# Performance work log

Hardware: AMD Instinct MI355X
Metric: run time of the kernel (lower is better)

## Reference

```python
import math
import jax, jax.numpy as jnp
import numpy as np

NP_, NA_ = 100000, 50000
IN_DIM = OUT_DIM = 128
H, DK = 4, 32
E_CITES, E_WRITES, E_REV = 600000, 300000, 300000


def setup_inputs() -> dict:
    key = jax.random.key(0)
    ks = jax.random.split(key, 16)
    s_in = 1.0 / math.sqrt(IN_DIM)   # ~ Linear default init scale
    s_dk = 1.0 / math.sqrt(DK)       # ~ xavier for d_k x d_k
    return {
        "h_paper": jax.random.normal(ks[0], (NP_, IN_DIM), jnp.float32),
        "h_author": jax.random.normal(ks[1], (NA_, IN_DIM), jnp.float32),
        "Wk": jax.random.normal(ks[2], (2, OUT_DIM, IN_DIM), jnp.float32) * s_in,
        "bk": jnp.zeros((2, OUT_DIM), jnp.float32),
        "Wq": jax.random.normal(ks[3], (2, OUT_DIM, IN_DIM), jnp.float32) * s_in,
        "bq": jnp.zeros((2, OUT_DIM), jnp.float32),
        "Wv": jax.random.normal(ks[4], (2, OUT_DIM, IN_DIM), jnp.float32) * s_in,
        "bv": jnp.zeros((2, OUT_DIM), jnp.float32),
        "Wa": jax.random.normal(ks[5], (2, OUT_DIM, OUT_DIM), jnp.float32) * s_in,
        "ba": jnp.zeros((2, OUT_DIM), jnp.float32),
        "rel_att": jax.random.normal(ks[6], (3, H, DK, DK), jnp.float32) * s_dk,
        "rel_msg": jax.random.normal(ks[7], (3, H, DK, DK), jnp.float32) * s_dk,
        "rel_pri": jnp.ones((3, H), jnp.float32),
        "skip": jnp.ones((2,), jnp.float32),
        "cites_src": jax.random.randint(ks[8], (E_CITES,), 0, NP_, jnp.int32),
        "cites_dst": jax.random.randint(ks[9], (E_CITES,), 0, NP_, jnp.int32),
        "writes_src": jax.random.randint(ks[10], (E_WRITES,), 0, NA_, jnp.int32),
        "writes_dst": jax.random.randint(ks[11], (E_WRITES,), 0, NP_, jnp.int32),
        "rev_src": jax.random.randint(ks[12], (E_REV,), 0, NP_, jnp.int32),
        "rev_dst": jax.random.randint(ks[13], (E_REV,), 0, NA_, jnp.int32),
    }


def _seg_softmax(scores, seg, n):
    # edge softmax normalized by destination node (DGL edge_softmax, norm_by='dst')
    m = jax.ops.segment_max(scores, seg, num_segments=n)
    e = jnp.exp(scores - m[seg])
    z = jax.ops.segment_sum(e, seg, num_segments=n)
    return e / z[seg]


def reference(h_paper, h_author, Wk, bk, Wq, bq, Wv, bv, Wa, ba,
              rel_att, rel_msg, rel_pri, skip,
              cites_src, cites_dst, writes_src, writes_dst, rev_src, rev_dst):
    sqrt_dk = math.sqrt(DK)

    def proj(h, W, b, t):
        return (h @ W[t].T + b[t]).reshape(-1, H, DK)  # [N, H, dk]

    def rel_agg(h_src, h_dst, ts, td, e, src, dst, n_dst):
        # relation-specific transforms of k and v (per-head dk x dk matmul)
        k = jnp.einsum('nhi,hij->nhj', proj(h_src, Wk, bk, ts), rel_att[e])
        v = jnp.einsum('nhi,hij->nhj', proj(h_src, Wv, bv, ts), rel_msg[e])
        q = proj(h_dst, Wq, bq, td)
        # per-edge attention logits: (q_dst . k_src) * pri / sqrt(dk)  -> [E, H]
        score = jnp.einsum('ehd,ehd->eh', q[dst], k[src]) * rel_pri[e] / sqrt_dk
        a = _seg_softmax(score, dst, n_dst)
        # weighted scatter-sum of messages to destination nodes
        return jax.ops.segment_sum(v[src] * a[:, :, None], dst, num_segments=n_dst)

    # cross_reducer='mean': average per-relation aggregates per dst node type
    t_paper = (rel_agg(h_paper, h_paper, 0, 0, 0, cites_src, cites_dst, NP_) +
               rel_agg(h_author, h_paper, 1, 0, 1, writes_src, writes_dst, NP_)) * 0.5
    t_author = rel_agg(h_paper, h_author, 0, 1, 2, rev_src, rev_dst, NA_)

    def out(t, h, nt):
        trans = t.reshape(-1, OUT_DIM) @ Wa[nt].T + ba[nt]  # dropout = identity (eval)
        alpha = jax.nn.sigmoid(skip[nt])
        return trans * alpha + h * (1.0 - alpha)

    return jnp.concatenate([out(t_paper, h_paper, 0), out(t_author, h_author, 1)], axis=0)
```

## Files before the change

### kernel.cpp

```cpp
#include <hip/hip_runtime.h>
#include <hip/hip_bf16.h>
#include <math.h>

#define NP 100000
#define NA 50000
#define DIM 128
#define NH 4
#define DKK 32
#define EC 600000
#define EW 300000
#define ER 300000
#define CAP 32
#define SCL 0.17677669529663687f

#define CDIV(a,b) (((a)+(b)-1)/(b))

typedef __attribute__((ext_vector_type(8))) short bf16x8;
typedef __attribute__((ext_vector_type(4))) float f32x4;
typedef __attribute__((ext_vector_type(2))) float f32x2;

__device__ __forceinline__ ushort f2b(float f){
  unsigned u = __float_as_uint(f);
  unsigned r = u + 0x7FFFu + ((u>>16)&1u);
  return (ushort)(r>>16);
}
__device__ __forceinline__ float blo(unsigned u){ return __uint_as_float(u<<16); }
__device__ __forceinline__ float bhi(unsigned u){ return __uint_as_float(u & 0xFFFF0000u); }

struct C2Args { const float4* in[2]; uint2* out[2]; };
__global__ void k_cast2(C2Args a){
  int s = blockIdx.y;
  int i = blockIdx.x*256 + threadIdx.x;
  float4 v = a.in[s][i];
  uint2 o;
  o.x = (unsigned)f2b(v.x) | ((unsigned)f2b(v.y)<<16);
  o.y = (unsigned)f2b(v.z) | ((unsigned)f2b(v.w)<<16);
  a.out[s][i] = o;
}

__global__ void k_zero_i(int* p, int n){
  int i = blockIdx.x*blockDim.x + threadIdx.x;
  if (i < n) p[i] = 0;
}

__global__ void k_fuse(const float* __restrict__ Wk, const float* __restrict__ bk,
                       const float* __restrict__ Wv, const float* __restrict__ bv,
                       const float* __restrict__ rel_att, const float* __restrict__ rel_msg,
                       ushort* __restrict__ Wfb_all, float* __restrict__ bfu_all){
  int rel = blockIdx.x >> 7;
  int ts = (rel==1) ? 1 : 0;
  ushort* Wfb = Wfb_all + rel*32768;
  float*  bfu = bfu_all + rel*256;
  int idx = (blockIdx.x & 127)*256 + threadIdx.x;
  int which = idx >> 14;
  int rem = idx & 16383;
  int op = rem >> 7;
  int j  = rem & 127;
  int h = op >> 5, jp = op & 31;
  const float* W  = which ? Wv : Wk;
  const float* R  = which ? rel_msg : rel_att;
  const float* Wt = W + (size_t)ts*DIM*DIM;
  const float* Re = R + (((size_t)rel*NH + h)*DKK)*DKK + jp;
  float acc = 0.f;
  #pragma unroll
  for (int i=0;i<DKK;i++) acc += Wt[(h*DKK+i)*DIM + j] * Re[(size_t)i*DKK];
  Wfb[which*16384 + op*DIM + j] = f2b(acc);
  if (idx < 256){
    int w2 = idx >> 7; int op2 = idx & 127; int h2 = op2>>5, jp2 = op2&31;
    const float* bsrc = (w2 ? bv : bk) + (size_t)ts*DIM;
    const float* R2 = (w2 ? rel_msg : rel_att) + (((size_t)rel*NH + h2)*DKK)*DKK + jp2;
    float accb = 0.f;
    #pragma unroll
    for (int i=0;i<DKK;i++) accb += bsrc[h2*DKK+i]*R2[(size_t)i*DKK];
    bfu[w2*DIM + op2] = accb;
  }
}

struct MArgs {
  const float* X[3];
  const ushort* W[3][3];
  const float* b[3][3];
  ushort* Y[3][3];
  int ystride[3][3];
  int N[3];
  int npan[3];
  int base[3];
};
__global__ __launch_bounds__(512) void k_mega(MArgs g){
  int b = blockIdx.x;
  int seg = (b >= g.base[2]) ? 2 : ((b >= g.base[1]) ? 1 : 0);
  int local = b - g.base[seg];
  int N = g.N[seg];
  int tile = local*64;
  if (tile >= N) return;
  int tid = threadIdx.x;
  int wv = tid >> 6, l = tid & 63;
  int lr = l & 15, lk = l >> 4;
  int rowg = wv >> 1, colg = wv & 1;
  int arow = tile + rowg*16 + lr;
  int ar = (arow < N) ? arow : 0;
  const float4* Ar = (const float4*)(g.X[seg] + (size_t)ar*DIM);
  bf16x8 A[4];
  #pragma unroll
  for (int kc=0;kc<4;kc++){
    float4 u = Ar[kc*8 + lk*2];
    float4 v = Ar[kc*8 + lk*2 + 1];
    bf16x8 a;
    a[0]=(short)f2b(u.x); a[1]=(short)f2b(u.y); a[2]=(short)f2b(u.z); a[3]=(short)f2b(u.w);
    a[4]=(short)f2b(v.x); a[5]=(short)f2b(v.y); a[6]=(short)f2b(v.z); a[7]=(short)f2b(v.w);
    A[kc] = a;
  }
  __shared__ __align__(16) ushort Wl[128*136];
  __shared__ __align__(16) ushort Ost[64*136];
  uint4* Wl4 = (uint4*)Wl;
  int npan = g.npan[seg];
  for (int p=0; p<npan; ++p){
    const uint4* Ws = (const uint4*)g.W[seg][p];
    #pragma unroll
    for (int i=0;i<4;i++){
      int idx = i*512 + tid;
      uint4 v = Ws[idx];
      int r = idx >> 4, c = idx & 15;
      Wl4[r*17 + c] = v;
    }
    __syncthreads();
    const float* bias = g.b[seg][p];
    #pragma unroll
    for (int ct=0; ct<4; ct++){
      int col = colg*64 + ct*16 + lr;
      f32x4 acc = {0.f,0.f,0.f,0.f};
      #pragma unroll
      for (int kc=0;kc<4;kc++){
        bf16x8 B = *(const bf16x8*)&Wl[col*136 + kc*32 + lk*8];
        acc = __builtin_amdgcn_mfma_f32_16x16x32_bf16(A[kc], B, acc, 0, 0, 0);
      }
      float bv = bias[col];
      #pragma unroll
      for (int j=0;j<4;j++)
        Ost[(rowg*16 + lk*4 + j)*136 + col] = f2b(acc[j] + bv);
    }
    __syncthreads();
    int orow = tid >> 3;
    int oseg = (tid & 7)*2;
    int grow = tile + orow;
    if (grow < N){
      uint4* dst = (uint4*)(g.Y[seg][p] + (size_t)grow*g.ystride[seg][p]);
      const uint4* s = (const uint4*)Ost;
      dst[oseg]   = s[orow*17 + oseg];
      dst[oseg+1] = s[orow*17 + oseg + 1];
    }
    __syncthreads();
  }
}

struct BArgs { const int* dst[3]; const int* src[3]; int* cnt[3]; int* slots[3]; int E[3]; int n[3]; };
__global__ void k_bucket(BArgs a){
  int r = blockIdx.y;
  int E = a.E[r], n = a.n[r];
  const int* dst = a.dst[r];
  const int* srcv = a.src[r];
  int* cnt = a.cnt[r];
  int* slots = a.slots[r];
  int g = blockIdx.x & 7;
  int sub = blockIdx.x >> 3;
  int chunk = (n + 7) >> 3;
  int lo = g*chunk;
  int hi = lo + chunk; if (hi > n) hi = n;
  int per = (E + 255) >> 8;
  per = (per + 3) & ~3;
  int e0 = sub*per;
  int e1 = e0 + per; if (e1 > E) e1 = E;
  for (int i = e0 + threadIdx.x*4; i < e1; i += 256*4){
    if (i + 4 <= e1){
      int4 d = *(const int4*)(dst + i);
      int4 s = *(const int4*)(srcv + i);
      if (d.x>=lo && d.x<hi){ int p=atomicAdd(&cnt[d.x],1); if(p<CAP) slots[(size_t)d.x*CAP+p]=s.x; }
      if (d.y>=lo && d.y<hi){ int p=atomicAdd(&cnt[d.y],1); if(p<CAP) slots[(size_t)d.y*CAP+p]=s.y; }
      if (d.z>=lo && d.z<hi){ int p=atomicAdd(&cnt[d.z],1); if(p<CAP) slots[(size_t)d.z*CAP+p]=s.z; }
      if (d.w>=lo && d.w<hi){ int p=atomicAdd(&cnt[d.w],1); if(p<CAP) slots[(size_t)d.w*CAP+p]=s.w; }
    } else {
      for (int j=i; j<e1; ++j){
        int d = dst[j];
        if (d>=lo && d<hi){ int p=atomicAdd(&cnt[d],1); if(p<CAP) slots[(size_t)d*CAP+p]=srcv[j]; }
      }
    }
  }
}

__device__ __forceinline__ void agg_step4(const unsigned* __restrict__ KV,
    const int4* __restrict__ sl4,
    int i, int deg, int nsrc, float qx, float qy, int lane,
    f32x2& av, float& z)
{
  int4 s4 = sl4[i>>2];
  int s0 = ((unsigned)s4.x < (unsigned)nsrc) ? s4.x : 0;
  int s1 = ((unsigned)s4.y < (unsigned)nsrc) ? s4.y : 0;
  int s2 = ((unsigned)s4.z < (unsigned)nsrc) ? s4.z : 0;
  int s3 = ((unsigned)s4.w < (unsigned)nsrc) ? s4.w : 0;
  bool v1 = (i+1 < deg), v2 = (i+2 < deg), v3 = (i+3 < deg);
  const unsigned* r0 = KV + (size_t)s0*128;
  const unsigned* r1 = KV + (size_t)s1*128;
  const unsigned* r2 = KV + (size_t)s2*128;
  const unsigned* r3 = KV + (size_t)s3*128;
  unsigned ku0 = r0[lane];
  unsigned ku1 = r1[lane];
  unsigned ku2 = r2[lane];
  unsigned ku3 = r3[lane];
  unsigned vu0 = r0[64 + lane];
  unsigned vu1 = r1[64 + lane];
  unsigned vu2 = r2[64 + lane];
  unsigned vu3 = r3[64 + lane];
  float p0 = qx*blo(ku0) + qy*bhi(ku0);
  float p1 = qx*blo(ku1) + qy*bhi(ku1);
  float p2 = qx*blo(ku2) + qy*bhi(ku2);
  float p3 = qx*blo(ku3) + qy*bhi(ku3);
  #pragma unroll
  for (int d=1; d<16; d<<=1){
    p0 += __shfl_xor(p0, d);
    p1 += __shfl_xor(p1, d);
    p2 += __shfl_xor(p2, d);
    p3 += __shfl_xor(p3, d);
  }
  float e0 = __expf(p0);
  float e1 = v1 ? __expf(p1) : 0.f;
  float e2 = v2 ? __expf(p2) : 0.f;
  float e3 = v3 ? __expf(p3) : 0.f;
  z += (e0+e1)+(e2+e3);
  f32x2 w0 = {blo(vu0), bhi(vu0)};
  f32x2 w1 = {blo(vu1), bhi(vu1)};
  f32x2 w2 = {blo(vu2), bhi(vu2)};
  f32x2 w3 = {blo(vu3), bhi(vu3)};
  av += (w0*e0 + w1*e1) + (w2*e2 + w3*e3);
}

struct AFArgs {
  const unsigned *QP, *QA, *KV0, *KV1, *KV2;
  const int *slots, *cnt;
  const float *pri;
  const ushort *WaP, *WaA;
  const float *baP, *baA;
  const float *hP, *hA;
  float *outP, *outA;
  const float *skip;
  int PB;
};
__global__ __launch_bounds__(512) void k_attnfin(AFArgs a){
  bool isP = (blockIdx.x < (unsigned)a.PB);
  int wbase = isP ? blockIdx.x*64 : (blockIdx.x - a.PB)*64;
  int N = isP ? NP : NA;
  int tid = threadIdx.x;
  int wid = tid >> 6;
  int lane = tid & 63;
  int h = lane >> 4;
  __shared__ float Ls[64][132];
  __shared__ int nextrow;
  if (tid == 0) nextrow = 0;
  __syncthreads();
  for (;;){
    int row;
    if (lane == 0) row = atomicAdd(&nextrow, 1);
    row = __shfl(row, 0);
    if (row >= 64) break;
    int w = wbase + row;
    if (w < N){
      f32x2 o;
      if (isP){
        unsigned qu = a.QP[(size_t)w*64 + lane];
        float qx = blo(qu), qy = bhi(qu);
        float s0f = a.pri[h]*SCL, s1f = a.pri[NH+h]*SCL;
        float qx0 = qx*s0f, qy0 = qy*s0f;
        float qx1 = qx*s1f, qy1 = qy*s1f;
        int d0 = a.cnt[w];      if (d0 > CAP) d0 = CAP;
        int d1 = a.cnt[NP + w]; if (d1 > CAP) d1 = CAP;
        const int4* sl0 = (const int4*)(a.slots + (size_t)w*CAP);
        const int4* sl1 = (const int4*)(a.slots + ((size_t)NP+w)*CAP);
        f32x2 x = {0.f,0.f}, y = {0.f,0.f};
        float zx = 0.f, zy = 0.f;
        int nmax = (d0 > d1) ? d0 : d1;
        for (int i = 0; i < nmax; i += 4){
          if (i < d0) agg_step4(a.KV0, sl0, i, d0, NP, qx0, qy0, lane, x, zx);
          if (i < d1) agg_step4(a.KV1, sl1, i, d1, NA, qx1, qy1, lane, y, zy);
        }
        float ix = (zx > 0.f) ? 1.f/zx : 0.f;
        float iy = (zy > 0.f) ? 1.f/zy : 0.f;
        o = x*ix + y*iy;
      } else {
        unsigned qu = a.QA[(size_t)w*64 + lane];
        float qx = blo(qu), qy = bhi(qu);
        float s2f = a.pri[2*NH+h]*SCL;
        float qx2 = qx*s2f, qy2 = qy*s2f;
        int d2 = a.cnt[2*NP + w]; if (d2 > CAP) d2 = CAP;
        const int4* sl2 = (const int4*)(a.slots + ((size_t)2*NP+w)*CAP);
        f32x2 r = {0.f,0.f};
        float zr = 0.f;
        for (int i = 0; i < d2; i += 4)
          agg_step4(a.KV2, sl2, i, d2, NP, qx2, qy2, lane, r, zr);
        float ir = (zr > 0.f) ? 1.f/zr : 0.f;
        o = r*ir;
      }
      *(f32x2*)&Ls[row][2*lane] = o;
    }
  }
  __syncthreads();
  const ushort* Wb  = isP ? a.WaP : a.WaA;
  const float* bias = isP ? a.baP : a.baA;
  const float* hin  = isP ? a.hP  : a.hA;
  float* out        = isP ? a.outP : a.outA;
  float scale       = isP ? 0.5f : 1.0f;
  float alpha = 1.f/(1.f + expf(-a.skip[isP ? 0 : 1]));
  float beta  = 1.f - alpha;
  int lr = lane & 15, lk = lane >> 4;
  int rowg = wid >> 1, colg = wid & 1;
  int r0loc = rowg*16;
  int c0 = colg*64;
  bf16x8 A[4];
  #pragma unroll
  for (int kc=0;kc<4;kc++){
    const float* src = &Ls[r0loc + lr][kc*32 + lk*8];
    bf16x8 aa;
    #pragma unroll
    for (int j=0;j<8;j++) aa[j] = (short)f2b(src[j]);
    A[kc] = aa;
  }
  __syncthreads();
  #pragma unroll
  for (int ct=0; ct<4; ct++){
    int col = c0 + ct*16 + lr;
    const bf16x8* Wrow = (const bf16x8*)(Wb + (size_t)col*DIM);
    f32x4 acc = {0.f,0.f,0.f,0.f};
    #pragma unroll
    for (int kc=0;kc<4;kc++)
      acc = __builtin_amdgcn_mfma_f32_16x16x32_bf16(A[kc], Wrow[kc*4+lk], acc, 0, 0, 0);
    float bv = bias[col];
    #pragma unroll
    for (int j=0;j<4;j++){
      int lrow = r0loc + lk*4 + j;
      Ls[lrow][col] = scale*acc[j] + bv;
    }
  }
  __syncthreads();
  int orow = tid >> 3;
  int ocb  = (tid & 7)*16;
  int row  = wbase + orow;
  if (row < N){
    const float4* H4 = (const float4*)hin;
    float4* O4 = (float4*)out;
    #pragma unroll
    for (int q=0;q<4;q++){
      float4 tv = *(const float4*)&Ls[orow][ocb + q*4];
      float4 hv = H4[(size_t)row*32 + (ocb>>2) + q];
      float4 o;
      o.x = alpha*tv.x + beta*hv.x;
      o.y = alpha*tv.y + beta*hv.y;
      o.z = alpha*tv.z + beta*hv.z;
      o.w = alpha*tv.w + beta*hv.w;
      O4[(size_t)row*32 + (ocb>>2) + q] = o;
    }
  }
}

extern "C" void kernel_launch(void* const* d_in, const int* in_sizes, int n_in,
                              void* d_out, int out_size, void* d_ws, size_t ws_size,
                              hipStream_t stream) {
  const float* h_paper = (const float*)d_in[0];
  const float* h_author= (const float*)d_in[1];
  const float* Wk = (const float*)d_in[2];
  const float* bk = (const float*)d_in[3];
  const float* Wq = (const float*)d_in[4];
  const float* bq = (const float*)d_in[5];
  const float* Wv = (const float*)d_in[6];
  const float* bv = (const float*)d_in[7];
  const float* Wa = (const float*)d_in[8];
  const float* ba = (const float*)d_in[9];
  const float* rel_att = (const float*)d_in[10];
  const float* rel_msg = (const float*)d_in[11];
  const float* rel_pri = (const float*)d_in[12];
  const float* skip    = (const float*)d_in[13];
  const int* cites_src = (const int*)d_in[14];
  const int* cites_dst = (const int*)d_in[15];
  const int* writes_src= (const int*)d_in[16];
  const int* writes_dst= (const int*)d_in[17];
  const int* rev_src   = (const int*)d_in[18];
  const int* rev_dst   = (const int*)d_in[19];

  ushort* qbP = (ushort*)d_ws;
  ushort* qbA = qbP + (size_t)NP*DIM;
  ushort* KV0 = qbA + (size_t)NA*DIM;
  ushort* KV1 = KV0 + (size_t)NP*256;
  ushort* KV2 = KV1 + (size_t)NA*256;
  ushort* Wqb = KV2 + (size_t)NP*256;
  ushort* Wab = Wqb + 32768;
  ushort* Wfb = Wab + 32768;
  float*  bfu = (float*)(Wfb + 3*32768);
  int* ib = (int*)(bfu + 3*256);
  const int NDST_TOT = 2*NP + NA;
  int* cnt_all   = ib;           ib += NDST_TOT;
  int* slots_all = ib;

  float* t_paper  = (float*)d_out;
  float* t_author = (float*)d_out + (size_t)NP*DIM;

  const int cntB[3] = {0, NP, 2*NP};

  {
    C2Args a;
    a.in[0]=(const float4*)Wq; a.out[0]=(uint2*)Wqb;
    a.in[1]=(const float4*)Wa; a.out[1]=(uint2*)Wab;
    k_cast2<<<dim3(32,2),256,0,stream>>>(a);
  }
  k_fuse<<<384,256,0,stream>>>(Wk, bk, Wv, bv, rel_att, rel_msg, Wfb, bfu);
  k_zero_i<<<CDIV(NDST_TOT,256),256,0,stream>>>(cnt_all, NDST_TOT);
  {
    BArgs b;
    const int* dsts[3] = {cites_dst, writes_dst, rev_dst};
    const int* srcs[3] = {cites_src, writes_src, rev_src};
    int Es[3] = {EC, EW, ER};
    int ns[3] = {NP, NP, NA};
    for (int r=0;r<3;r++){
      b.dst[r]=dsts[r]; b.src[r]=srcs[r];
      b.cnt[r]=cnt_all+cntB[r];
      b.slots[r]=slots_all+(size_t)cntB[r]*CAP;
      b.E[r]=Es[r]; b.n[r]=ns[r];
    }
    k_bucket<<<dim3(2048,3),256,0,stream>>>(b);
  }
  {
    const int T0 = CDIV(NP,64), T1 = CDIV(NA,64), T2 = CDIV(NP,64);
    MArgs m;
    m.base[0]=0; m.base[1]=T0; m.base[2]=T0+T1;
    m.X[0]=h_paper;  m.N[0]=NP; m.npan[0]=3;
    m.W[0][0]=Wqb;        m.b[0][0]=bq;        m.Y[0][0]=qbP;      m.ystride[0][0]=128;
    m.W[0][1]=Wfb;        m.b[0][1]=bfu;       m.Y[0][1]=KV0;      m.ystride[0][1]=256;
    m.W[0][2]=Wfb+16384;  m.b[0][2]=bfu+DIM;   m.Y[0][2]=KV0+128;  m.ystride[0][2]=256;
    m.X[1]=h_author; m.N[1]=NA; m.npan[1]=3;
    m.W[1][0]=Wqb+16384;        m.b[1][0]=bq+DIM;        m.Y[1][0]=qbA;      m.ystride[1][0]=128;
    m.W[1][1]=Wfb+32768;        m.b[1][1]=bfu+256;       m.Y[1][1]=KV1;      m.ystride[1][1]=256;
    m.W[1][2]=Wfb+32768+16384;  m.b[1][2]=bfu+256+DIM;   m.Y[1][2]=KV1+128;  m.ystride[1][2]=256;
    m.X[2]=h_paper;  m.N[2]=NP; m.npan[2]=2;
    m.W[2][0]=Wfb+2*32768;        m.b[2][0]=bfu+512;       m.Y[2][0]=KV2;      m.ystride[2][0]=256;
    m.W[2][1]=Wfb+2*32768+16384;  m.b[2][1]=bfu+512+DIM;   m.Y[2][1]=KV2+128;  m.ystride[2][1]=256;
    m.W[2][2]=Wfb;                m.b[2][2]=bfu;           m.Y[2][2]=KV2;      m.ystride[2][2]=256;
    k_mega<<<T0+T1+T2,512,0,stream>>>(m);
  }
  {
    const int PB = CDIV(NP,64);
    const int AB = CDIV(NA,64);
    AFArgs a;
    a.QP = (const unsigned*)qbP;  a.QA = (const unsigned*)qbA;
    a.KV0 = (const unsigned*)KV0; a.KV1 = (const unsigned*)KV1; a.KV2 = (const unsigned*)KV2;
    a.slots = slots_all; a.cnt = cnt_all;
    a.pri = rel_pri;
    a.WaP = Wab; a.WaA = Wab + 16384;
    a.baP = ba;  a.baA = ba + DIM;
    a.hP = h_paper; a.hA = h_author;
    a.outP = t_paper; a.outA = t_author;
    a.skip = skip;
    a.PB = PB;
    k_attnfin<<<PB+AB,512,0,stream>>>(a);
  }
}
```

Baseline: 327.0 us.

## Merge setup kernels and co-schedule edge bucketing with projection GEMMs

The weight cast, weight fusion and counter-zeroing kernels are combined into one launch. Edge bucketing is folded into the projection GEMM launch as extra blocks, so the atomic-bound scatter work can overlap with the MFMA projection tiles. This cuts kernel launch count and the serialization between independent stages. The cost is a larger, heterogeneous grid where bucketing blocks use 512 threads with a different edge partition, and they may compete with the GEMM blocks for CU resources.

```diff
diff --git a/kernel.cpp b/kernel.cpp
--- a/kernel.cpp
+++ b/kernel.cpp
@@ -27,56 +27,61 @@
 __device__ __forceinline__ float blo(unsigned u){ return __uint_as_float(u<<16); }
 __device__ __forceinline__ float bhi(unsigned u){ return __uint_as_float(u & 0xFFFF0000u); }
 
-struct C2Args { const float4* in[2]; uint2* out[2]; };
-__global__ void k_cast2(C2Args a){
-  int s = blockIdx.y;
-  int i = blockIdx.x*256 + threadIdx.x;
-  float4 v = a.in[s][i];
-  uint2 o;
-  o.x = (unsigned)f2b(v.x) | ((unsigned)f2b(v.y)<<16);
-  o.y = (unsigned)f2b(v.z) | ((unsigned)f2b(v.w)<<16);
-  a.out[s][i] = o;
-}
-
-__global__ void k_zero_i(int* p, int n){
-  int i = blockIdx.x*blockDim.x + threadIdx.x;
-  if (i < n) p[i] = 0;
-}
-
-__global__ void k_fuse(const float* __restrict__ Wk, const float* __restrict__ bk,
-                       const float* __restrict__ Wv, const float* __restrict__ bv,
-                       const float* __restrict__ rel_att, const float* __restrict__ rel_msg,
-                       ushort* __restrict__ Wfb_all, float* __restrict__ bfu_all){
-  int rel = blockIdx.x >> 7;
-  int ts = (rel==1) ? 1 : 0;
-  ushort* Wfb = Wfb_all + rel*32768;
-  float*  bfu = bfu_all + rel*256;
-  int idx = (blockIdx.x & 127)*256 + threadIdx.x;
-  int which = idx >> 14;
-  int rem = idx & 16383;
-  int op = rem >> 7;
-  int j  = rem & 127;
-  int h = op >> 5, jp = op & 31;
-  const float* W  = which ? Wv : Wk;
-  const float* R  = which ? rel_msg : rel_att;
-  const float* Wt = W + (size_t)ts*DIM*DIM;
-  const float* Re = R + (((size_t)rel*NH + h)*DKK)*DKK + jp;
-  float acc = 0.f;
-  #pragma unroll
-  for (int i=0;i<DKK;i++) acc += Wt[(h*DKK+i)*DIM + j] * Re[(size_t)i*DKK];
-  Wfb[which*16384 + op*DIM + j] = f2b(acc);
-  if (idx < 256){
-    int w2 = idx >> 7; int op2 = idx & 127; int h2 = op2>>5, jp2 = op2&31;
-    const float* bsrc = (w2 ? bv : bk) + (size_t)ts*DIM;
-    const float* R2 = (w2 ? rel_msg : rel_att) + (((size_t)rel*NH + h2)*DKK)*DKK + jp2;
-    float accb = 0.f;
-    #pragma unroll
-    for (int i=0;i<DKK;i++) accb += bsrc[h2*DKK+i]*R2[(size_t)i*DKK];
-    bfu[w2*DIM + op2] = accb;
-  }
-}
-
-struct MArgs {
+struct PreArgs {
+  const float4* wqin; uint2* wqout;
+  const float4* wain; uint2* waout;
+  const float *Wk, *bk, *Wv, *bv, *rel_att, *rel_msg;
+  ushort* Wfb_all; float* bfu_all;
+  int* cnt; int ncnt;
+};
+__global__ void k_pre(PreArgs a){
+  int b = blockIdx.x;
+  int tid = threadIdx.x;
+  if (b < 64){
+    const float4* in = (b < 32) ? a.wqin : a.wain;
+    uint2* out = (b < 32) ? a.wqout : a.waout;
+    int i = (b & 31)*256 + tid;
+    float4 v = in[i];
+    uint2 o;
+    o.x = (unsigned)f2b(v.x) | ((unsigned)f2b(v.y)<<16);
+    o.y = (unsigned)f2b(v.z) | ((unsigned)f2b(v.w)<<16);
+    out[i] = o;
+  } else if (b < 448){
+    int fb = b - 64;
+    int rel = fb >> 7;
+    int ts = (rel==1) ? 1 : 0;
+    ushort* Wfb = a.Wfb_all + rel*32768;
+    float*  bfu = a.bfu_all + rel*256;
+    int idx = (fb & 127)*256 + tid;
+    int which = idx >> 14;
+    int rem = idx & 16383;
+    int op = rem >> 7;
+    int j  = rem & 127;
+    int h = op >> 5, jp = op & 31;
+    const float* W  = which ? a.Wv : a.Wk;
+    const float* R  = which ? a.rel_msg : a.rel_att;
+    const float* Wt = W + (size_t)ts*DIM*DIM;
+    const float* Re = R + (((size_t)rel*NH + h)*DKK)*DKK + jp;
+    float acc = 0.f;
+    #pragma unroll
+    for (int i=0;i<DKK;i++) acc += Wt[(h*DKK+i)*DIM + j] * Re[(size_t)i*DKK];
+    Wfb[which*16384 + op*DIM + j] = f2b(acc);
+    if (idx < 256){
+      int w2 = idx >> 7; int op2 = idx & 127; int h2 = op2>>5, jp2 = op2&31;
+      const float* bsrc = (w2 ? a.bv : a.bk) + (size_t)ts*DIM;
+      const float* R2 = (w2 ? a.rel_msg : a.rel_att) + (((size_t)rel*NH + h2)*DKK)*DKK + jp2;
+      float accb = 0.f;
+      #pragma unroll
+      for (int i=0;i<DKK;i++) accb += bsrc[h2*DKK+i]*R2[(size_t)i*DKK];
+      bfu[w2*DIM + op2] = accb;
+    }
+  } else {
+    int i = (b - 448)*256 + tid;
+    if (i < a.ncnt) a.cnt[i] = 0;
+  }
+}
+
+struct CArgs {
   const float* X[3];
   const ushort* W[3][3];
   const float* b[3][3];
@@ -85,15 +90,57 @@
   int N[3];
   int npan[3];
   int base[3];
+  int MT;
+  const int* dst[3];
+  const int* src[3];
+  int* cnt[3];
+  int* slots[3];
+  int E[3];
+  int n[3];
 };
-__global__ __launch_bounds__(512) void k_mega(MArgs g){
+__global__ __launch_bounds__(512) void k_combo(CArgs g){
+  int tid = threadIdx.x;
+  if ((int)blockIdx.x >= g.MT){
+    int bb = blockIdx.x - g.MT;
+    int r = bb >> 10;
+    int lb = bb & 1023;
+    int E = g.E[r], n = g.n[r];
+    const int* dst = g.dst[r];
+    const int* srcv = g.src[r];
+    int* cnt = g.cnt[r];
+    int* slots = g.slots[r];
+    int grp = lb & 7;
+    int sub = lb >> 3;
+    int chunk = (n + 7) >> 3;
+    int lo = grp*chunk;
+    int hi = lo + chunk; if (hi > n) hi = n;
+    int per = (E + 127) >> 7;
+    per = (per + 3) & ~3;
+    int e0 = sub*per;
+    int e1 = e0 + per; if (e1 > E) e1 = E;
+    for (int i = e0 + tid*4; i < e1; i += 512*4){
+      if (i + 4 <= e1){
+        int4 d = *(const int4*)(dst + i);
+        int4 s = *(const int4*)(srcv + i);
+        if (d.x>=lo && d.x<hi){ int p=atomicAdd(&cnt[d.x],1); if(p<CAP) slots[(size_t)d.x*CAP+p]=s.x; }
+        if (d.y>=lo && d.y<hi){ int p=atomicAdd(&cnt[d.y],1); if(p<CAP) slots[(size_t)d.y*CAP+p]=s.y; }
+        if (d.z>=lo && d.z<hi){ int p=atomicAdd(&cnt[d.z],1); if(p<CAP) slots[(size_t)d.z*CAP+p]=s.z; }
+        if (d.w>=lo && d.w<hi){ int p=atomicAdd(&cnt[d.w],1); if(p<CAP) slots[(size_t)d.w*CAP+p]=s.w; }
+      } else {
+        for (int j=i; j<e1; ++j){
+          int d = dst[j];
+          if (d>=lo && d<hi){ int p=atomicAdd(&cnt[d],1); if(p<CAP) slots[(size_t)d*CAP+p]=srcv[j]; }
+        }
+      }
+    }
+    return;
+  }
   int b = blockIdx.x;
   int seg = (b >= g.base[2]) ? 2 : ((b >= g.base[1]) ? 1 : 0);
   int local = b - g.base[seg];
   int N = g.N[seg];
   int tile = local*64;
   if (tile >= N) return;
-  int tid = threadIdx.x;
   int wv = tid >> 6, l = tid & 63;
   int lr = l & 15, lk = l >> 4;
   int rowg = wv >> 1, colg = wv & 1;
@@ -120,8 +167,7 @@
     for (int i=0;i<4;i++){
       int idx = i*512 + tid;
       uint4 v = Ws[idx];
-      int r = idx >> 4, c = idx & 15;
-      Wl4[r*17 + c] = v;
+      Wl4[(idx>>4)*17 + (idx&15)] = v;
     }
     __syncthreads();
     const float* bias = g.b[seg][p];
@@ -150,40 +196,6 @@
       dst[oseg+1] = s[orow*17 + oseg + 1];
     }
     __syncthreads();
-  }
-}
-
-struct BArgs { const int* dst[3]; const int* src[3]; int* cnt[3]; int* slots[3]; int E[3]; int n[3]; };
-__global__ void k_bucket(BArgs a){
-  int r = blockIdx.y;
-  int E = a.E[r], n = a.n[r];
-  const int* dst = a.dst[r];
-  const int* srcv = a.src[r];
-  int* cnt = a.cnt[r];
-  int* slots = a.slots[r];
-  int g = blockIdx.x & 7;
-  int sub = blockIdx.x >> 3;
-  int chunk = (n + 7) >> 3;
-  int lo = g*chunk;
-  int hi = lo + chunk; if (hi > n) hi = n;
-  int per = (E + 255) >> 8;
-  per = (per + 3) & ~3;
-  int e0 = sub*per;
-  int e1 = e0 + per; if (e1 > E) e1 = E;
-  for (int i = e0 + threadIdx.x*4; i < e1; i += 256*4){
-    if (i + 4 <= e1){
-      int4 d = *(const int4*)(dst + i);
-      int4 s = *(const int4*)(srcv + i);
-      if (d.x>=lo && d.x<hi){ int p=atomicAdd(&cnt[d.x],1); if(p<CAP) slots[(size_t)d.x*CAP+p]=s.x; }
-      if (d.y>=lo && d.y<hi){ int p=atomicAdd(&cnt[d.y],1); if(p<CAP) slots[(size_t)d.y*CAP+p]=s.y; }
-      if (d.z>=lo && d.z<hi){ int p=atomicAdd(&cnt[d.z],1); if(p<CAP) slots[(size_t)d.z*CAP+p]=s.z; }
-      if (d.w>=lo && d.w<hi){ int p=atomicAdd(&cnt[d.w],1); if(p<CAP) slots[(size_t)d.w*CAP+p]=s.w; }
-    } else {
-      for (int j=i; j<e1; ++j){
-        int d = dst[j];
-        if (d>=lo && d<hi){ int p=atomicAdd(&cnt[d],1); if(p<CAP) slots[(size_t)d*CAP+p]=srcv[j]; }
-      }
-    }
   }
 }
 
@@ -403,44 +415,43 @@
   const int cntB[3] = {0, NP, 2*NP};
 
   {
-    C2Args a;
-    a.in[0]=(const float4*)Wq; a.out[0]=(uint2*)Wqb;
-    a.in[1]=(const float4*)Wa; a.out[1]=(uint2*)Wab;
-    k_cast2<<<dim3(32,2),256,0,stream>>>(a);
-  }
-  k_fuse<<<384,256,0,stream>>>(Wk, bk, Wv, bv, rel_att, rel_msg, Wfb, bfu);
-  k_zero_i<<<CDIV(NDST_TOT,256),256,0,stream>>>(cnt_all, NDST_TOT);
+    PreArgs p;
+    p.wqin = (const float4*)Wq; p.wqout = (uint2*)Wqb;
+    p.wain = (const float4*)Wa; p.waout = (uint2*)Wab;
+    p.Wk = Wk; p.bk = bk; p.Wv = Wv; p.bv = bv;
+    p.rel_att = rel_att; p.rel_msg = rel_msg;
+    p.Wfb_all = Wfb; p.bfu_all = bfu;
+    p.cnt = cnt_all; p.ncnt = NDST_TOT;
+    k_pre<<<448 + CDIV(NDST_TOT,256),256,0,stream>>>(p);
+  }
   {
-    BArgs b;
+    const int T0 = CDIV(NP,64), T1 = CDIV(NA,64), T2 = CDIV(NP,64);
+    const int MT = T0+T1+T2;
+    CArgs c;
+    c.base[0]=0; c.base[1]=T0; c.base[2]=T0+T1; c.MT = MT;
+    c.X[0]=h_paper;  c.N[0]=NP; c.npan[0]=3;
+    c.W[0][0]=Wqb;        c.b[0][0]=bq;        c.Y[0][0]=qbP;      c.ystride[0][0]=128;
+    c.W[0][1]=Wfb;        c.b[0][1]=bfu;       c.Y[0][1]=KV0;      c.ystride[0][1]=256;
+    c.W[0][2]=Wfb+16384;  c.b[0][2]=bfu+DIM;   c.Y[0][2]=KV0+128;  c.ystride[0][2]=256;
+    c.X[1]=h_author; c.N[1]=NA; c.npan[1]=3;
+    c.W[1][0]=Wqb+16384;        c.b[1][0]=bq+DIM;        c.Y[1][0]=qbA;      c.ystride[1][0]=128;
+    c.W[1][1]=Wfb+32768;        c.b[1][1]=bfu+256;       c.Y[1][1]=KV1;      c.ystride[1][1]=256;
+    c.W[1][2]=Wfb+32768+16384;  c.b[1][2]=bfu+256+DIM;   c.Y[1][2]=KV1+128;  c.ystride[1][2]=256;
+    c.X[2]=h_paper;  c.N[2]=NP; c.npan[2]=2;
+    c.W[2][0]=Wfb+2*32768;        c.b[2][0]=bfu+512;       c.Y[2][0]=KV2;      c.ystride[2][0]=256;
+    c.W[2][1]=Wfb+2*32768+16384;  c.b[2][1]=bfu+512+DIM;   c.Y[2][1]=KV2+128;  c.ystride[2][1]=256;
+    c.W[2][2]=Wfb;                c.b[2][2]=bfu;           c.Y[2][2]=KV2;      c.ystride[2][2]=256;
     const int* dsts[3] = {cites_dst, writes_dst, rev_dst};
     const int* srcs[3] = {cites_src, writes_src, rev_src};
     int Es[3] = {EC, EW, ER};
     int ns[3] = {NP, NP, NA};
     for (int r=0;r<3;r++){
-      b.dst[r]=dsts[r]; b.src[r]=srcs[r];
-      b.cnt[r]=cnt_all+cntB[r];
-      b.slots[r]=slots_all+(size_t)cntB[r]*CAP;
-      b.E[r]=Es[r]; b.n[r]=ns[r];
-    }
-    k_bucket<<<dim3(2048,3),256,0,stream>>>(b);
-  }
-  {
-    const int T0 = CDIV(NP,64), T1 = CDIV(NA,64), T2 = CDIV(NP,64);
-    MArgs m;
-    m.base[0]=0; m.base[1]=T0; m.base[2]=T0+T1;
-    m.X[0]=h_paper;  m.N[0]=NP; m.npan[0]=3;
-    m.W[0][0]=Wqb;        m.b[0][0]=bq;        m.Y[0][0]=qbP;      m.ystride[0][0]=128;
-    m.W[0][1]=Wfb;        m.b[0][1]=bfu;       m.Y[0][1]=KV0;      m.ystride[0][1]=256;
-    m.W[0][2]=Wfb+16384;  m.b[0][2]=bfu+DIM;   m.Y[0][2]=KV0+128;  m.ystride[0][2]=256;
-    m.X[1]=h_author; m.N[1]=NA; m.npan[1]=3;
-    m.W[1][0]=Wqb+16384;        m.b[1][0]=bq+DIM;        m.Y[1][0]=qbA;      m.ystride[1][0]=128;
-    m.W[1][1]=Wfb+32768;        m.b[1][1]=bfu+256;       m.Y[1][1]=KV1;      m.ystride[1][1]=256;
-    m.W[1][2]=Wfb+32768+16384;  m.b[1][2]=bfu+256+DIM;   m.Y[1][2]=KV1+128;  m.ystride[1][2]=256;
-    m.X[2]=h_paper;  m.N[2]=NP; m.npan[2]=2;
-    m.W[2][0]=Wfb+2*32768;        m.b[2][0]=bfu+512;       m.Y[2][0]=KV2;      m.ystride[2][0]=256;
-    m.W[2][1]=Wfb+2*32768+16384;  m.b[2][1]=bfu+512+DIM;   m.Y[2][1]=KV2+128;  m.ystride[2][1]=256;
-    m.W[2][2]=Wfb;                m.b[2][2]=bfu;           m.Y[2][2]=KV2;      m.ystride[2][2]=256;
-    k_mega<<<T0+T1+T2,512,0,stream>>>(m);
+      c.dst[r]=dsts[r]; c.src[r]=srcs[r];
+      c.cnt[r]=cnt_all+cntB[r];
+      c.slots[r]=slots_all+(size_t)cntB[r]*CAP;
+      c.E[r]=Es[r]; c.n[r]=ns[r];
+    }
+    k_combo<<<MT + 3*1024,512,0,stream>>>(c);
   }
   {
     const int PB = CDIV(NP,64);
```

Result: faster. 309.7 us (-5.3%).
